# Performance work log

Hardware: AMD Instinct MI355X
Metric: run time of the kernel (lower is better)

Reference implementation:

```python
import jax, jax.numpy as jnp
import numpy as np

SUPPORT_FACTOR = 2.5
EPSILON = 1e-5


def setup_inputs() -> dict:
    key = jax.random.key(0)
    k1, _ = jax.random.split(key)
    # 64x64 regular particle grid on [0,1]^2 -> N = 4096 nodes
    n_side = 64
    g = jnp.linspace(0.0, 1.0, n_side, dtype=jnp.float32)
    gx, gy = jnp.meshgrid(g, g, indexing='ij')
    nodes = jnp.stack([gx.ravel(), gy.ravel()], axis=-1)  # [4096, 2]
    # B = 4096 query (collocation) points inside the same domain
    x = jax.random.uniform(k1, (4096, 2), dtype=jnp.float32)
    return {"x": x, "nodes": nodes}


def _cubic_spline(q):
    # piecewise cubic spline kernel; zero outside q > 1
    w_inner = 2.0 / 3.0 - 4.0 * q ** 2 + 4.0 * q ** 3          # q <= 0.5
    w_outer = 4.0 / 3.0 - 4.0 * q + 4.0 * q ** 2 - (4.0 / 3.0) * q ** 3  # 0.5 < q <= 1
    return jnp.where(q <= 0.5, w_inner, jnp.where(q <= 1.0, w_outer, 0.0))


def _dilation(nodes):
    # support_factor * mean nearest-neighbor spacing (replaces init-time cKDTree)
    d2 = jnp.sum((nodes[:, None, :] - nodes[None, :, :]) ** 2, axis=-1)  # [N, N]
    d2 = d2 + jnp.where(jnp.eye(nodes.shape[0], dtype=bool), jnp.inf, 0.0)
    h_avg = jnp.mean(jnp.sqrt(jnp.min(d2, axis=1)))
    return SUPPORT_FACTOR * h_avg


def reference(x, nodes):
    dilation = _dilation(nodes)
    diff = x[:, None, :] - nodes[None, :, :]          # [B, N, 2]
    dx = diff[..., 0]
    dy = diff[..., 1]
    dist = jnp.sqrt(dx ** 2 + dy ** 2 + 1e-10)        # [B, N]
    q = dist / dilation
    w = _cubic_spline(q) * (q <= 1.0)                 # support-radius mask
    ones = jnp.ones_like(dx)
    P = jnp.stack([ones, dx, dy], axis=-1)            # [B, N, 3]
    M = jnp.einsum('bni,bnj,bn->bij', P, P, w)        # [B, 3, 3] moment matrices
    M_reg = M + jnp.eye(3, dtype=x.dtype) * EPSILON
    M_inv = jnp.linalg.inv(M_reg)                     # batched 3x3 inverse
    P_w = P * w[..., None]
    b_vec = jnp.einsum('bij,bnj->bni', M_inv, P_w)    # [B, N, 3]
    phi = b_vec[..., 0]
    phi_x = -b_vec[..., 1]
    phi_y = -b_vec[..., 2]
    return (phi, phi_x, phi_y)
```

## Files before the change

kernel.cpp:

```cpp
#include <hip/hip_runtime.h>

#define N_NODES 4096
#define B_PTS   4096
#define SUPPORT_FACTOR 2.5f
#define EPSILON 1e-5f

__global__ __launch_bounds__(256) void nearest_kernel(
        const float* __restrict__ nodes, float* __restrict__ mind) {
    const int i = blockIdx.x;
    const float xi = nodes[2 * i];
    const float yi = nodes[2 * i + 1];

    const float4* nodes4 = (const float4*)nodes;
    float mind2 = 3.4e38f;
    for (int k = threadIdx.x; k < N_NODES / 2; k += 256) {
        float4 v = nodes4[k];
        float dx0 = xi - v.x, dy0 = yi - v.y;
        float dx1 = xi - v.z, dy1 = yi - v.w;
        float d20 = dx0 * dx0 + dy0 * dy0;
        float d21 = dx1 * dx1 + dy1 * dy1;
        if (2 * k != i)     mind2 = fminf(mind2, d20);
        if (2 * k + 1 != i) mind2 = fminf(mind2, d21);
    }
    #pragma unroll
    for (int off = 32; off > 0; off >>= 1)
        mind2 = fminf(mind2, __shfl_down(mind2, off, 64));

    __shared__ float sw[4];
    const int wave = threadIdx.x >> 6;
    if ((threadIdx.x & 63) == 0) sw[wave] = mind2;
    __syncthreads();
    if (threadIdx.x == 0) {
        float m = fminf(fminf(sw[0], sw[1]), fminf(sw[2], sw[3]));
        mind[i] = sqrtf(m);
    }
}

__global__ __launch_bounds__(256) void dil_reduce_kernel(
        const float* __restrict__ mind, float* __restrict__ dsum) {
    float s = 0.f;
    const float4* m4 = (const float4*)mind;
    for (int k = threadIdx.x; k < N_NODES / 4; k += 256) {
        float4 v = m4[k];
        s += (v.x + v.y) + (v.z + v.w);
    }
    #pragma unroll
    for (int off = 32; off > 0; off >>= 1)
        s += __shfl_down(s, off, 64);
    __shared__ float sw[4];
    const int wave = threadIdx.x >> 6;
    if ((threadIdx.x & 63) == 0) sw[wave] = s;
    __syncthreads();
    if (threadIdx.x == 0)
        *dsum = (sw[0] + sw[1] + sw[2] + sw[3]) * (SUPPORT_FACTOR / (float)N_NODES);
}

__device__ __forceinline__ float cubic_w(float q) {
    if (q <= 0.5f) return 2.0f / 3.0f + q * q * (4.0f * q - 4.0f);
    if (q <= 1.0f) return 4.0f / 3.0f + q * (-4.0f + q * (4.0f - (4.0f / 3.0f) * q));
    return 0.0f;
}

__global__ __launch_bounds__(256) void rkpm_kernel(
        const float* __restrict__ x, const float* __restrict__ nodes,
        const float* __restrict__ dsum, float* __restrict__ out) {
    __shared__ float sx[N_NODES];
    __shared__ float sy[N_NODES];
    __shared__ float sred[4][6];
    __shared__ float sminv[9];

    const int b = blockIdx.x;
    const int tid = threadIdx.x;

    const float2* nodes2 = (const float2*)nodes;
    for (int j = tid; j < N_NODES; j += 256) {
        float2 nd = nodes2[j];
        sx[j] = nd.x;
        sy[j] = nd.y;
    }

    const float2 xq = ((const float2*)x)[b];
    const float xb = xq.x;
    const float yb = xq.y;
    const float inv_dil = 1.0f / (*dsum);
    __syncthreads();

    const float4* sx4 = (const float4*)sx;
    const float4* sy4 = (const float4*)sy;

    float wreg[16];
    float m00 = 0.f, m01 = 0.f, m02 = 0.f, m11 = 0.f, m12 = 0.f, m22 = 0.f;
    #pragma unroll
    for (int kk = 0; kk < 4; ++kk) {
        const int idx = kk * 256 + tid;
        float4 xs = sx4[idx];
        float4 ys = sy4[idx];
        #pragma unroll
        for (int c = 0; c < 4; ++c) {
            float nx = (c == 0) ? xs.x : (c == 1) ? xs.y : (c == 2) ? xs.z : xs.w;
            float ny = (c == 0) ? ys.x : (c == 1) ? ys.y : (c == 2) ? ys.z : ys.w;
            float dx = xb - nx;
            float dy = yb - ny;
            float dist = sqrtf(dx * dx + dy * dy + 1e-10f);
            float w = cubic_w(dist * inv_dil);
            wreg[kk * 4 + c] = w;
            m00 += w;
            m01 += w * dx;
            m02 += w * dy;
            m11 += w * dx * dx;
            m12 += w * dx * dy;
            m22 += w * dy * dy;
        }
    }
    #pragma unroll
    for (int off = 32; off > 0; off >>= 1) {
        m00 += __shfl_down(m00, off, 64);
        m01 += __shfl_down(m01, off, 64);
        m02 += __shfl_down(m02, off, 64);
        m11 += __shfl_down(m11, off, 64);
        m12 += __shfl_down(m12, off, 64);
        m22 += __shfl_down(m22, off, 64);
    }
    const int wave = tid >> 6;
    if ((tid & 63) == 0) {
        sred[wave][0] = m00; sred[wave][1] = m01; sred[wave][2] = m02;
        sred[wave][3] = m11; sred[wave][4] = m12; sred[wave][5] = m22;
    }
    __syncthreads();

    if (tid == 0) {
        float a  = sred[0][0] + sred[1][0] + sred[2][0] + sred[3][0] + EPSILON;
        float bb = sred[0][1] + sred[1][1] + sred[2][1] + sred[3][1];
        float c  = sred[0][2] + sred[1][2] + sred[2][2] + sred[3][2];
        float d  = sred[0][3] + sred[1][3] + sred[2][3] + sred[3][3] + EPSILON;
        float e  = sred[0][4] + sred[1][4] + sred[2][4] + sred[3][4];
        float f  = sred[0][5] + sred[1][5] + sred[2][5] + sred[3][5] + EPSILON;
        float c00 = d * f - e * e;
        float c01 = c * e - bb * f;
        float c02 = bb * e - c * d;
        float det = a * c00 + bb * c01 + c * c02;
        float idet = 1.0f / det;
        float i00 = c00 * idet;
        float i01 = c01 * idet;
        float i02 = c02 * idet;
        float i11 = (a * f - c * c) * idet;
        float i12 = (bb * c - a * e) * idet;
        float i22 = (a * d - bb * bb) * idet;
        sminv[0] = i00;  sminv[1] = i01;  sminv[2] = i02;
        sminv[3] = -i01; sminv[4] = -i11; sminv[5] = -i12;
        sminv[6] = -i02; sminv[7] = -i12; sminv[8] = -i22;
    }
    __syncthreads();

    const float i00 = sminv[0], i01 = sminv[1], i02 = sminv[2];
    const float n01 = sminv[3], n11 = sminv[4], n12 = sminv[5];
    const float n02 = sminv[6], n12b = sminv[7], n22 = sminv[8];

    const size_t BN = (size_t)B_PTS * N_NODES;
    float4* __restrict__ out_phi = (float4*)(out + (size_t)b * N_NODES);
    float4* __restrict__ out_px  = (float4*)(out + BN + (size_t)b * N_NODES);
    float4* __restrict__ out_py  = (float4*)(out + 2 * BN + (size_t)b * N_NODES);

    #pragma unroll
    for (int kk = 0; kk < 4; ++kk) {
        const int idx = kk * 256 + tid;
        float4 xs = sx4[idx];
        float4 ys = sy4[idx];
        float4 ph, px, py;
        #pragma unroll
        for (int c = 0; c < 4; ++c) {
            float nx = (c == 0) ? xs.x : (c == 1) ? xs.y : (c == 2) ? xs.z : xs.w;
            float ny = (c == 0) ? ys.x : (c == 1) ? ys.y : (c == 2) ? ys.z : ys.w;
            float dx = xb - nx;
            float dy = yb - ny;
            float w = wreg[kk * 4 + c];
            float vph = w * (i00 + i01 * dx + i02 * dy);
            float vpx = w * (n01 + n11 * dx + n12 * dy);
            float vpy = w * (n02 + n12b * dx + n22 * dy);
            if (c == 0) { ph.x = vph; px.x = vpx; py.x = vpy; }
            else if (c == 1) { ph.y = vph; px.y = vpx; py.y = vpy; }
            else if (c == 2) { ph.z = vph; px.z = vpx; py.z = vpy; }
            else { ph.w = vph; px.w = vpx; py.w = vpy; }
        }
        out_phi[idx] = ph;
        out_px[idx]  = px;
        out_py[idx]  = py;
    }
}

extern "C" void kernel_launch(void* const* d_in, const int* in_sizes, int n_in,
                              void* d_out, int out_size, void* d_ws, size_t ws_size,
                              hipStream_t stream) {
    const float* x     = (const float*)d_in[0];
    const float* nodes = (const float*)d_in[1];
    float* out  = (float*)d_out;
    float* mind = (float*)d_ws;
    float* dsum = mind + N_NODES;

    nearest_kernel<<<N_NODES, 256, 0, stream>>>(nodes, mind);
    dil_reduce_kernel<<<1, 256, 0, stream>>>(mind, dsum);
    rkpm_kernel<<<B_PTS, 256, 0, stream>>>(x, nodes, dsum, out);
}
```

Baseline: 212.4 us.

## Fuse dilation reduction into RKPM kernel and drop shared-memory node staging

Removes the single-block dilation reduction kernel; each RKPM block now re-reduces the 4096 nearest distances itself. Nodes are read directly from global memory (cached in L2) instead of staged through 32KB of LDS, and dx/dy are kept in registers for the output pass. Launch bounds now request 4 blocks per CU. The aim is to cut a launch, the LDS staging cost and its occupancy limit, in exchange for redundant per-block reduction work and more register pressure.

```diff
diff --git a/kernel.cpp b/kernel.cpp
--- a/kernel.cpp
+++ b/kernel.cpp
@@ -36,74 +36,63 @@
     }
 }
 
-__global__ __launch_bounds__(256) void dil_reduce_kernel(
-        const float* __restrict__ mind, float* __restrict__ dsum) {
-    float s = 0.f;
-    const float4* m4 = (const float4*)mind;
-    for (int k = threadIdx.x; k < N_NODES / 4; k += 256) {
-        float4 v = m4[k];
-        s += (v.x + v.y) + (v.z + v.w);
-    }
-    #pragma unroll
-    for (int off = 32; off > 0; off >>= 1)
-        s += __shfl_down(s, off, 64);
-    __shared__ float sw[4];
-    const int wave = threadIdx.x >> 6;
-    if ((threadIdx.x & 63) == 0) sw[wave] = s;
-    __syncthreads();
-    if (threadIdx.x == 0)
-        *dsum = (sw[0] + sw[1] + sw[2] + sw[3]) * (SUPPORT_FACTOR / (float)N_NODES);
-}
-
 __device__ __forceinline__ float cubic_w(float q) {
     if (q <= 0.5f) return 2.0f / 3.0f + q * q * (4.0f * q - 4.0f);
     if (q <= 1.0f) return 4.0f / 3.0f + q * (-4.0f + q * (4.0f - (4.0f / 3.0f) * q));
     return 0.0f;
 }
 
-__global__ __launch_bounds__(256) void rkpm_kernel(
+__global__ __launch_bounds__(256, 4) void rkpm_kernel(
         const float* __restrict__ x, const float* __restrict__ nodes,
-        const float* __restrict__ dsum, float* __restrict__ out) {
-    __shared__ float sx[N_NODES];
-    __shared__ float sy[N_NODES];
+        const float* __restrict__ mind, float* __restrict__ out) {
     __shared__ float sred[4][6];
-    __shared__ float sminv[9];
+    __shared__ float sbc[10];
 
     const int b = blockIdx.x;
     const int tid = threadIdx.x;
+    const int wave = tid >> 6;
+    const int lane = tid & 63;
 
-    const float2* nodes2 = (const float2*)nodes;
-    for (int j = tid; j < N_NODES; j += 256) {
-        float2 nd = nodes2[j];
-        sx[j] = nd.x;
-        sy[j] = nd.y;
+    const float4* m4 = (const float4*)mind;
+    float s = 0.f;
+    #pragma unroll
+    for (int k = 0; k < 4; ++k) {
+        float4 v = m4[k * 256 + tid];
+        s += (v.x + v.y) + (v.z + v.w);
     }
+    #pragma unroll
+    for (int off = 32; off > 0; off >>= 1)
+        s += __shfl_down(s, off, 64);
+    if (lane == 0) sred[wave][0] = s;
+    __syncthreads();
+    if (tid == 0) {
+        float dil = (sred[0][0] + sred[1][0] + sred[2][0] + sred[3][0]) *
+                    (SUPPORT_FACTOR / (float)N_NODES);
+        sbc[0] = 1.0f / dil;
+    }
+    __syncthreads();
+    const float inv_dil = sbc[0];
 
     const float2 xq = ((const float2*)x)[b];
-    const float xb = xq.x;
-    const float yb = xq.y;
-    const float inv_dil = 1.0f / (*dsum);
-    __syncthreads();
+    const float xb = xq.x, yb = xq.y;
 
-    const float4* sx4 = (const float4*)sx;
-    const float4* sy4 = (const float4*)sy;
-
-    float wreg[16];
+    const float4* nodes4 = (const float4*)nodes;
+    float wr[16], dxr[16], dyr[16];
     float m00 = 0.f, m01 = 0.f, m02 = 0.f, m11 = 0.f, m12 = 0.f, m22 = 0.f;
     #pragma unroll
     for (int kk = 0; kk < 4; ++kk) {
-        const int idx = kk * 256 + tid;
-        float4 xs = sx4[idx];
-        float4 ys = sy4[idx];
+        float4 va = nodes4[kk * 512 + 2 * tid];
+        float4 vb = nodes4[kk * 512 + 2 * tid + 1];
         #pragma unroll
         for (int c = 0; c < 4; ++c) {
-            float nx = (c == 0) ? xs.x : (c == 1) ? xs.y : (c == 2) ? xs.z : xs.w;
-            float ny = (c == 0) ? ys.x : (c == 1) ? ys.y : (c == 2) ? ys.z : ys.w;
+            float nx = (c == 0) ? va.x : (c == 1) ? va.z : (c == 2) ? vb.x : vb.z;
+            float ny = (c == 0) ? va.y : (c == 1) ? va.w : (c == 2) ? vb.y : vb.w;
             float dx = xb - nx;
             float dy = yb - ny;
             float dist = sqrtf(dx * dx + dy * dy + 1e-10f);
             float w = cubic_w(dist * inv_dil);
-            wreg[kk * 4 + c] = w;
+            const int r = kk * 4 + c;
+            wr[r] = w; dxr[r] = dx; dyr[r] = dy;
             m00 += w;
             m01 += w * dx;
             m02 += w * dy;
@@ -121,8 +110,7 @@
         m12 += __shfl_down(m12, off, 64);
         m22 += __shfl_down(m22, off, 64);
     }
-    const int wave = tid >> 6;
-    if ((tid & 63) == 0) {
+    if (lane == 0) {
         sred[wave][0] = m00; sred[wave][1] = m01; sred[wave][2] = m02;
         sred[wave][3] = m11; sred[wave][4] = m12; sred[wave][5] = m22;
     }
@@ -146,15 +134,15 @@
         float i11 = (a * f - c * c) * idet;
         float i12 = (bb * c - a * e) * idet;
         float i22 = (a * d - bb * bb) * idet;
-        sminv[0] = i00;  sminv[1] = i01;  sminv[2] = i02;
-        sminv[3] = -i01; sminv[4] = -i11; sminv[5] = -i12;
-        sminv[6] = -i02; sminv[7] = -i12; sminv[8] = -i22;
+        sbc[1] = i00;  sbc[2] = i01;  sbc[3] = i02;
+        sbc[4] = -i01; sbc[5] = -i11; sbc[6] = -i12;
+        sbc[7] = -i02; sbc[8] = -i12; sbc[9] = -i22;
     }
     __syncthreads();
 
-    const float i00 = sminv[0], i01 = sminv[1], i02 = sminv[2];
-    const float n01 = sminv[3], n11 = sminv[4], n12 = sminv[5];
-    const float n02 = sminv[6], n12b = sminv[7], n22 = sminv[8];
+    const float i00 = sbc[1], i01 = sbc[2], i02 = sbc[3];
+    const float n01 = sbc[4], n11 = sbc[5], n12 = sbc[6];
+    const float n02 = sbc[7], n12b = sbc[8], n22 = sbc[9];
 
     const size_t BN = (size_t)B_PTS * N_NODES;
     float4* __restrict__ out_phi = (float4*)(out + (size_t)b * N_NODES);
@@ -163,25 +151,20 @@
 
     #pragma unroll
     for (int kk = 0; kk < 4; ++kk) {
-        const int idx = kk * 256 + tid;
-        float4 xs = sx4[idx];
-        float4 ys = sy4[idx];
         float4 ph, px, py;
         #pragma unroll
         for (int c = 0; c < 4; ++c) {
-            float nx = (c == 0) ? xs.x : (c == 1) ? xs.y : (c == 2) ? xs.z : xs.w;
-            float ny = (c == 0) ? ys.x : (c == 1) ? ys.y : (c == 2) ? ys.z : ys.w;
-            float dx = xb - nx;
-            float dy = yb - ny;
-            float w = wreg[kk * 4 + c];
+            const int r = kk * 4 + c;
+            float w = wr[r], dx = dxr[r], dy = dyr[r];
             float vph = w * (i00 + i01 * dx + i02 * dy);
             float vpx = w * (n01 + n11 * dx + n12 * dy);
             float vpy = w * (n02 + n12b * dx + n22 * dy);
-            if (c == 0) { ph.x = vph; px.x = vpx; py.x = vpy; }
+            if (c == 0)      { ph.x = vph; px.x = vpx; py.x = vpy; }
             else if (c == 1) { ph.y = vph; px.y = vpx; py.y = vpy; }
             else if (c == 2) { ph.z = vph; px.z = vpx; py.z = vpy; }
-            else { ph.w = vph; px.w = vpx; py.w = vpy; }
+            else             { ph.w = vph; px.w = vpx; py.w = vpy; }
         }
+        const int idx = kk * 256 + tid;
         out_phi[idx] = ph;
         out_px[idx]  = px;
         out_py[idx]  = py;
@@ -195,9 +178,7 @@
     const float* nodes = (const float*)d_in[1];
     float* out  = (float*)d_out;
     float* mind = (float*)d_ws;
-    float* dsum = mind + N_NODES;
 
     nearest_kernel<<<N_NODES, 256, 0, stream>>>(nodes, mind);
-    dil_reduce_kernel<<<1, 256, 0, stream>>>(mind, dsum);
-    rkpm_kernel<<<B_PTS, 256, 0, stream>>>(x, nodes, dsum, out);
+    rkpm_kernel<<<B_PTS, 256, 0, stream>>>(x, nodes, mind, out);
 }
```

After: 209.1 us (median of 2 runs). Within noise of the previous version (-1.5%).
